# Performance work log

Measured on AMD Instinct MI355X. Metric: run time of the kernel, lower is better.

Reference implementation:

```python
import jax, jax.numpy as jnp
import numpy as np

HIDDEN = 2048
NUM_EXPERTS = 64
TOP_K = 8
EPS = 1e-6


def setup_inputs() -> dict:
    key = jax.random.key(0)
    k1, k2, k3, k4 = jax.random.split(key, 4)
    hidden_states = jax.random.normal(k1, (4, 4096, HIDDEN), dtype=jnp.float32)
    scale = jnp.ones((HIDDEN,), dtype=jnp.float32) + 0.01 * jax.random.normal(k2, (HIDDEN,), dtype=jnp.float32)
    proj_w = jax.random.normal(k3, (NUM_EXPERTS, HIDDEN), dtype=jnp.float32) * (HIDDEN ** -0.5)
    per_expert_scale = jnp.ones((NUM_EXPERTS,), dtype=jnp.float32) + 0.01 * jax.random.normal(k4, (NUM_EXPERTS,), dtype=jnp.float32)
    return {"hidden_states": hidden_states, "scale": scale, "proj_w": proj_w, "per_expert_scale": per_expert_scale}


def reference(hidden_states, scale, proj_w, per_expert_scale):
    H = hidden_states.shape[-1]
    # RMSNorm without learned scale
    x = hidden_states * jax.lax.rsqrt(jnp.mean(hidden_states * hidden_states, axis=-1, keepdims=True) + EPS)
    # elementwise scale and 1/sqrt(H) root-size scaling
    x = x * scale * (H ** -0.5)
    # router logits: [B,S,E]
    logits = jnp.einsum("bsh,eh->bse", x, proj_w)
    router_probs = jax.nn.softmax(logits.astype(jnp.float32), axis=-1)
    top_k_weights, top_k_index = jax.lax.top_k(router_probs, TOP_K)
    top_k_weights = top_k_weights / jnp.sum(top_k_weights, axis=-1, keepdims=True)
    top_k_weights = top_k_weights * per_expert_scale[top_k_index]
    # histc with bins=E, min=0, max=E on integer indices == bincount
    num_tokens_per_expert = jnp.bincount(top_k_index.reshape(-1), length=NUM_EXPERTS).astype(jnp.float32)
    return (top_k_weights.astype(hidden_states.dtype), top_k_index, num_tokens_per_expert)
```

## Files before the change

### kernel.cpp

```cpp
#include <hip/hip_runtime.h>
#include <math.h>

#define HIDDEN   2048
#define NEXPERT  64
#define TOPK     8
#define TILEK    64
#define LDSTR    68
#define RSQRT_H  0.02209708691207961f
#define NTOK     16384
#define EPW      4

__global__ __launch_bounds__(256) void prep_wt4(
    const float* __restrict__ w, const float* __restrict__ scale,
    float* __restrict__ wt4)
{
    int i  = blockIdx.x * 256 + threadIdx.x;
    int ep = i & 3;
    int k  = (i >> 2) & (HIDDEN - 1);
    int eg = i >> 13;
    wt4[i] = w[(eg * EPW + ep) * HIDDEN + k] * scale[k] * RSQRT_H;
}

__global__ __launch_bounds__(1024) void router_main(
    const float* __restrict__ h, const float* __restrict__ wt4,
    const float* __restrict__ pes,
    float* __restrict__ out_w, float* __restrict__ out_i, float* __restrict__ out_c)
{
    __shared__ float lds[2 * 64 * LDSTR];

    const int tid  = (int)threadIdx.x;
    const int wave = __builtin_amdgcn_readfirstlane(tid >> 6);
    const int lane = tid & 63;
    const int t0   = (int)blockIdx.x * 64;

    const int tt = tid >> 4;
    const int kk = (tid & 15) * 4;
    const float* __restrict__ hload = h + (size_t)(t0 + tt) * HIDDEN + kk;
    const int wtt = tt * LDSTR + kk;
    const int rdo = lane * LDSTR;

    const float* __restrict__ wbase = wt4 + (size_t)wave * (HIDDEN * EPW);

    double accd[EPW];
#pragma unroll
    for (int e = 0; e < EPW; ++e) accd[e] = 0.0;
    float ssl = 0.f;

    float4 v = *(const float4*)hload;

    for (int tile = 0; tile < HIDDEN / TILEK; ++tile) {
        float* buf = &lds[(tile & 1) * (64 * LDSTR)];
        *(float4*)(&buf[wtt]) = v;
        ssl = fmaf(v.x, v.x, ssl);
        ssl = fmaf(v.y, v.y, ssl);
        ssl = fmaf(v.z, v.z, ssl);
        ssl = fmaf(v.w, v.w, ssl);
        __syncthreads();
        if (tile < HIDDEN / TILEK - 1)
            v = *(const float4*)(hload + (tile + 1) * TILEK);

        const float* __restrict__ wk0 = wbase + tile * (TILEK * EPW);
        float acc[EPW];
#pragma unroll
        for (int e = 0; e < EPW; ++e) acc[e] = 0.f;
#pragma unroll
        for (int k4 = 0; k4 < TILEK; k4 += 4) {
            float4 h4 = *(const float4*)(&buf[rdo + k4]);
            const float* __restrict__ wk = wk0 + k4 * EPW;
#pragma unroll
            for (int e = 0; e < EPW; ++e) acc[e] = fmaf(wk[e],           h4.x, acc[e]);
#pragma unroll
            for (int e = 0; e < EPW; ++e) acc[e] = fmaf(wk[EPW + e],     h4.y, acc[e]);
#pragma unroll
            for (int e = 0; e < EPW; ++e) acc[e] = fmaf(wk[2 * EPW + e], h4.z, acc[e]);
#pragma unroll
            for (int e = 0; e < EPW; ++e) acc[e] = fmaf(wk[3 * EPW + e], h4.w, acc[e]);
        }
#pragma unroll
        for (int e = 0; e < EPW; ++e) accd[e] += (double)acc[e];
    }

    ssl += __shfl_xor(ssl, 1, 16);
    ssl += __shfl_xor(ssl, 2, 16);
    ssl += __shfl_xor(ssl, 4, 16);
    ssl += __shfl_xor(ssl, 8, 16);

    __syncthreads();
    float* lg   = lds;
    float* lss  = lds + 64 * 65;
    int*   hist = (int*)(lds + 64 * 65 + 64);
    if ((tid & 15) == 0) lss[tt] = ssl;
    if (tid < NEXPERT) hist[tid] = 0;
    __syncthreads();

    {
        float s = lss[lane];
        float r = (float)(1.0 / sqrt((double)s * (1.0 / (double)HIDDEN) + 1e-6));
#pragma unroll
        for (int e = 0; e < EPW; ++e)
            lg[lane * 65 + wave * EPW + e] = (float)accd[e] * r;
    }
    __syncthreads();

    for (int i = 0; i < 4; ++i) {
        const int tok = wave * 4 + i;
        float logit = lg[tok * 65 + lane];

        float work = logit;
        float myval = 0.f; int myidx = 0; float m0 = 0.f;
#pragma unroll
        for (int j = 0; j < TOPK; ++j) {
            float mx = work;
#pragma unroll
            for (int off = 32; off; off >>= 1) mx = fmaxf(mx, __shfl_xor(mx, off, 64));
            unsigned long long msk = __ballot(work == mx);
            int src = __ffsll((long long)msk) - 1;
            if (j == 0) m0 = mx;
            if (lane == j) { myval = mx; myidx = src; }
            if (lane == src) work = -3.402823466e38f;
        }

        float ev = (lane < TOPK) ? expf(myval - m0) : 0.f;
        float es = ev;
        es += __shfl_xor(es, 1, 64);
        es += __shfl_xor(es, 2, 64);
        es += __shfl_xor(es, 4, 64);
        if (lane < TOPK) {
            float wgt = (ev / es) * pes[myidx];
            size_t o = (size_t)(t0 + tok) * TOPK + lane;
            out_w[o] = wgt;
            out_i[o] = (float)myidx;
            atomicAdd(&hist[myidx], 1);
        }
    }

    __syncthreads();
    if (tid < NEXPERT)
        atomicAdd(&out_c[tid], (float)hist[tid]);
}

extern "C" void kernel_launch(void* const* d_in, const int* in_sizes, int n_in,
                              void* d_out, int out_size, void* d_ws, size_t ws_size,
                              hipStream_t stream) {
    const float* h     = (const float*)d_in[0];
    const float* scale = (const float*)d_in[1];
    const float* w     = (const float*)d_in[2];
    const float* pes   = (const float*)d_in[3];

    float* wt4 = (float*)d_ws;

    float* out_w = (float*)d_out;
    float* out_i = (float*)d_out + (size_t)NTOK * TOPK;
    float* out_c = (float*)d_out + (size_t)NTOK * TOPK * 2;

    hipMemsetAsync(out_c, 0, NEXPERT * sizeof(float), stream);

    prep_wt4<<<(NEXPERT * HIDDEN) / 256, 256, 0, stream>>>(w, scale, wt4);

    router_main<<<NTOK / 64, 1024, 0, stream>>>(h, wt4, pes, out_w, out_i, out_c);
}
```

Measured before the change: 254.8 us.

## Compute router logits with split-fp16 MFMA instead of scalar FP32 FMAs

Replaces the scalar FP32 FMA router GEMM with MFMA 16x16x32 f16 instructions. Both activations and weights are split into high and low fp16 parts, and three MFMAs per tile (hh, hl, lh) approximate fp32 precision. Blocks shrink to 16 tokens and 256 threads with a double-buffered LDS staging of converted activations. Each wave handles a K-slice, and the partial sums are reduced across waves through LDS before top-k. This removes the ALU-bound FMA cost so the kernel becomes bound by HBM reads of the hidden states. The trade-off is conversion overhead and a small precision change that could flip near-tie top-k selections.

```diff
diff --git a/kernel.cpp b/kernel.cpp
--- a/kernel.cpp
+++ b/kernel.cpp
@@ -4,107 +4,168 @@
 #define HIDDEN   2048
 #define NEXPERT  64
 #define TOPK     8
-#define TILEK    64
-#define LDSTR    68
-#define RSQRT_H  0.02209708691207961f
 #define NTOK     16384
-#define EPW      4
-
-__global__ __launch_bounds__(256) void prep_wt4(
+#define TOKB     16
+#define CHUNK    256
+#define NCHUNK   8
+#define ROWP     264
+#define RSQRT_H  0.02209708691207961
+#define WSCALE   64.0f
+
+typedef __attribute__((ext_vector_type(8))) _Float16 v8h;
+typedef __attribute__((ext_vector_type(4))) float    v4f;
+
+static __device__ __forceinline__ unsigned short f16b(float x) {
+    return __builtin_bit_cast(unsigned short, (_Float16)x);
+}
+static __device__ __forceinline__ float f16f(unsigned short u) {
+    return (float)__builtin_bit_cast(_Float16, u);
+}
+
+__global__ __launch_bounds__(256) void prep_wf(
     const float* __restrict__ w, const float* __restrict__ scale,
-    float* __restrict__ wt4)
+    unsigned short* __restrict__ wf)
 {
-    int i  = blockIdx.x * 256 + threadIdx.x;
-    int ep = i & 3;
-    int k  = (i >> 2) & (HIDDEN - 1);
-    int eg = i >> 13;
-    wt4[i] = w[(eg * EPW + ep) * HIDDEN + k] * scale[k] * RSQRT_H;
-}
-
-__global__ __launch_bounds__(1024) void router_main(
-    const float* __restrict__ h, const float* __restrict__ wt4,
+    int i    = blockIdx.x * 256 + threadIdx.x;
+    int j    = i & 7;
+    int lane = (i >> 3) & 63;
+    int nt   = (i >> 9) & 3;
+    int ks   = i >> 11;
+    int e    = nt * 16 + (lane & 15);
+    int k    = ks * 32 + (lane >> 4) * 8 + j;
+    float v  = w[e * HIDDEN + k] * scale[k] * WSCALE;
+    unsigned short vh = f16b(v);
+    unsigned short vl = f16b(v - f16f(vh));
+    size_t base = (((size_t)(ks * 4 + nt) * 2) * 64 + lane) * 8 + j;
+    wf[base]       = vh;
+    wf[base + 512] = vl;
+}
+
+__global__ __launch_bounds__(256, 4) void router_main(
+    const float* __restrict__ h, const unsigned short* __restrict__ wf,
     const float* __restrict__ pes,
     float* __restrict__ out_w, float* __restrict__ out_i, float* __restrict__ out_c)
 {
-    __shared__ float lds[2 * 64 * LDSTR];
+    __shared__ __align__(16) char smem[34112];
+    unsigned short* Xb0 = (unsigned short*)smem;
+    float* lss = (float*)(smem + 33792);
+    int*   hist = (int*)(smem + 33856);
+    float* lg  = (float*)smem;
 
     const int tid  = (int)threadIdx.x;
-    const int wave = __builtin_amdgcn_readfirstlane(tid >> 6);
+    const int w    = __builtin_amdgcn_readfirstlane(tid >> 6);
     const int lane = tid & 63;
-    const int t0   = (int)blockIdx.x * 64;
-
-    const int tt = tid >> 4;
-    const int kk = (tid & 15) * 4;
-    const float* __restrict__ hload = h + (size_t)(t0 + tt) * HIDDEN + kk;
-    const int wtt = tt * LDSTR + kk;
-    const int rdo = lane * LDSTR;
-
-    const float* __restrict__ wbase = wt4 + (size_t)wave * (HIDDEN * EPW);
-
-    double accd[EPW];
-#pragma unroll
-    for (int e = 0; e < EPW; ++e) accd[e] = 0.0;
-    float ssl = 0.f;
-
-    float4 v = *(const float4*)hload;
-
-    for (int tile = 0; tile < HIDDEN / TILEK; ++tile) {
-        float* buf = &lds[(tile & 1) * (64 * LDSTR)];
-        *(float4*)(&buf[wtt]) = v;
-        ssl = fmaf(v.x, v.x, ssl);
-        ssl = fmaf(v.y, v.y, ssl);
-        ssl = fmaf(v.z, v.z, ssl);
-        ssl = fmaf(v.w, v.w, ssl);
+    const int m    = lane & 15;
+    const int quad = lane >> 4;
+    const int t0   = (int)blockIdx.x * TOKB;
+
+    if (tid < NEXPERT) hist[tid] = 0;
+
+    const int aoff = m * ROWP + quad * 8;
+
+    v4f acc[4];
+#pragma unroll
+    for (int nt = 0; nt < 4; ++nt) acc[nt] = (v4f)0.f;
+    float ss[4] = {0.f, 0.f, 0.f, 0.f};
+    float4 st[4];
+
+#pragma unroll
+    for (int i = 0; i < 4; ++i) {
+        int idx = i * 256 + tid, t = idx >> 6, kq = idx & 63;
+        st[i] = *(const float4*)(h + (size_t)(t0 + t) * HIDDEN + kq * 4);
+    }
+#pragma unroll
+    for (int i = 0; i < 4; ++i) {
+        int idx = i * 256 + tid, t = idx >> 6, kq = idx & 63;
+        float4 v = st[i];
+        ss[i] = fmaf(v.x, v.x, fmaf(v.y, v.y, fmaf(v.z, v.z, fmaf(v.w, v.w, ss[i]))));
+        unsigned short h0 = f16b(v.x), h1 = f16b(v.y), h2 = f16b(v.z), h3 = f16b(v.w);
+        unsigned short l0 = f16b(v.x - f16f(h0)), l1 = f16b(v.y - f16f(h1));
+        unsigned short l2 = f16b(v.z - f16f(h2)), l3 = f16b(v.w - f16f(h3));
+        uint2 hp = make_uint2((unsigned)h0 | ((unsigned)h1 << 16),
+                              (unsigned)h2 | ((unsigned)h3 << 16));
+        uint2 lp = make_uint2((unsigned)l0 | ((unsigned)l1 << 16),
+                              (unsigned)l2 | ((unsigned)l3 << 16));
+        *(uint2*)(&Xb0[t * ROWP + kq * 4])        = hp;
+        *(uint2*)(&Xb0[4224 + t * ROWP + kq * 4]) = lp;
+    }
+
+    for (int c = 0; c < NCHUNK; ++c) {
         __syncthreads();
-        if (tile < HIDDEN / TILEK - 1)
-            v = *(const float4*)(hload + (tile + 1) * TILEK);
-
-        const float* __restrict__ wk0 = wbase + tile * (TILEK * EPW);
-        float acc[EPW];
-#pragma unroll
-        for (int e = 0; e < EPW; ++e) acc[e] = 0.f;
-#pragma unroll
-        for (int k4 = 0; k4 < TILEK; k4 += 4) {
-            float4 h4 = *(const float4*)(&buf[rdo + k4]);
-            const float* __restrict__ wk = wk0 + k4 * EPW;
-#pragma unroll
-            for (int e = 0; e < EPW; ++e) acc[e] = fmaf(wk[e],           h4.x, acc[e]);
-#pragma unroll
-            for (int e = 0; e < EPW; ++e) acc[e] = fmaf(wk[EPW + e],     h4.y, acc[e]);
-#pragma unroll
-            for (int e = 0; e < EPW; ++e) acc[e] = fmaf(wk[2 * EPW + e], h4.z, acc[e]);
-#pragma unroll
-            for (int e = 0; e < EPW; ++e) acc[e] = fmaf(wk[3 * EPW + e], h4.w, acc[e]);
-        }
-#pragma unroll
-        for (int e = 0; e < EPW; ++e) accd[e] += (double)acc[e];
-    }
-
-    ssl += __shfl_xor(ssl, 1, 16);
-    ssl += __shfl_xor(ssl, 2, 16);
-    ssl += __shfl_xor(ssl, 4, 16);
-    ssl += __shfl_xor(ssl, 8, 16);
-
+        unsigned short* buf = Xb0 + (c & 1) * 8448;
+        unsigned short* nbuf = Xb0 + ((c + 1) & 1) * 8448;
+
+        if (c < NCHUNK - 1) {
+#pragma unroll
+            for (int i = 0; i < 4; ++i) {
+                int idx = i * 256 + tid, t = idx >> 6, kq = idx & 63;
+                st[i] = *(const float4*)(h + (size_t)(t0 + t) * HIDDEN
+                                           + (c + 1) * CHUNK + kq * 4);
+            }
+        }
+
+#pragma unroll
+        for (int s = 0; s < 2; ++s) {
+            const int ksl = 2 * w + s;
+            const int ksg = c * 8 + ksl;
+            v8h ah = *(const v8h*)(&buf[aoff + ksl * 32]);
+            v8h al = *(const v8h*)(&buf[4224 + aoff + ksl * 32]);
+#pragma unroll
+            for (int nt = 0; nt < 4; ++nt) {
+                const unsigned short* bp =
+                    wf + (((size_t)(ksg * 4 + nt) * 2) * 64 + lane) * 8;
+                v8h bh = *(const v8h*)bp;
+                v8h bl = *(const v8h*)(bp + 512);
+                acc[nt] = __builtin_amdgcn_mfma_f32_16x16x32_f16(ah, bh, acc[nt], 0, 0, 0);
+                acc[nt] = __builtin_amdgcn_mfma_f32_16x16x32_f16(ah, bl, acc[nt], 0, 0, 0);
+                acc[nt] = __builtin_amdgcn_mfma_f32_16x16x32_f16(al, bh, acc[nt], 0, 0, 0);
+            }
+        }
+
+        if (c < NCHUNK - 1) {
+#pragma unroll
+            for (int i = 0; i < 4; ++i) {
+                int idx = i * 256 + tid, t = idx >> 6, kq = idx & 63;
+                float4 v = st[i];
+                ss[i] = fmaf(v.x, v.x, fmaf(v.y, v.y, fmaf(v.z, v.z, fmaf(v.w, v.w, ss[i]))));
+                unsigned short h0 = f16b(v.x), h1 = f16b(v.y), h2 = f16b(v.z), h3 = f16b(v.w);
+                unsigned short l0 = f16b(v.x - f16f(h0)), l1 = f16b(v.y - f16f(h1));
+                unsigned short l2 = f16b(v.z - f16f(h2)), l3 = f16b(v.w - f16f(h3));
+                uint2 hp = make_uint2((unsigned)h0 | ((unsigned)h1 << 16),
+                                      (unsigned)h2 | ((unsigned)h3 << 16));
+                uint2 lp = make_uint2((unsigned)l0 | ((unsigned)l1 << 16),
+                                      (unsigned)l2 | ((unsigned)l3 << 16));
+                *(uint2*)(&nbuf[t * ROWP + kq * 4])        = hp;
+                *(uint2*)(&nbuf[4224 + t * ROWP + kq * 4]) = lp;
+            }
+        }
+    }
+
+#pragma unroll
+    for (int i = 0; i < 4; ++i) {
+        float s = ss[i];
+#pragma unroll
+        for (int off = 32; off; off >>= 1) s += __shfl_xor(s, off, 64);
+        if (lane == 0) lss[i * 4 + w] = s;
+    }
     __syncthreads();
-    float* lg   = lds;
-    float* lss  = lds + 64 * 65;
-    int*   hist = (int*)(lds + 64 * 65 + 64);
-    if ((tid & 15) == 0) lss[tt] = ssl;
-    if (tid < NEXPERT) hist[tid] = 0;
+
+#pragma unroll
+    for (int nt = 0; nt < 4; ++nt)
+#pragma unroll
+        for (int r = 0; r < 4; ++r) {
+            int tl = quad * 4 + r;
+            lg[(w * 16 + tl) * 65 + nt * 16 + m] = acc[nt][r];
+        }
     __syncthreads();
 
-    {
-        float s = lss[lane];
-        float r = (float)(1.0 / sqrt((double)s * (1.0 / (double)HIDDEN) + 1e-6));
-#pragma unroll
-        for (int e = 0; e < EPW; ++e)
-            lg[lane * 65 + wave * EPW + e] = (float)accd[e] * r;
-    }
-    __syncthreads();
-
-    for (int i = 0; i < 4; ++i) {
-        const int tok = wave * 4 + i;
-        float logit = lg[tok * 65 + lane];
+    for (int i = 0; i < 4; ++i) {
+        const int tok = w * 4 + i;
+        float lsum = (lg[tok * 65 + lane]          + lg[1040 + tok * 65 + lane])
+                   + (lg[2080 + tok * 65 + lane]   + lg[3120 + tok * 65 + lane]);
+        double sst = (double)lss[tok];
+        double rr  = 1.0 / sqrt(sst * (1.0 / (double)HIDDEN) + 1e-6);
+        float logit = (float)((double)lsum * rr * (RSQRT_H / (double)WSCALE));
 
         float work = logit;
         float myval = 0.f; int myidx = 0; float m0 = 0.f;
@@ -147,7 +208,7 @@
     const float* w     = (const float*)d_in[2];
     const float* pes   = (const float*)d_in[3];
 
-    float* wt4 = (float*)d_ws;
+    unsigned short* wf = (unsigned short*)d_ws;
 
     float* out_w = (float*)d_out;
     float* out_i = (float*)d_out + (size_t)NTOK * TOPK;
@@ -155,7 +216,7 @@
 
     hipMemsetAsync(out_c, 0, NEXPERT * sizeof(float), stream);
 
-    prep_wt4<<<(NEXPERT * HIDDEN) / 256, 256, 0, stream>>>(w, scale, wt4);
-
-    router_main<<<NTOK / 64, 1024, 0, stream>>>(h, wt4, pes, out_w, out_i, out_c);
-}
+    prep_wf<<<512, 256, 0, stream>>>(w, scale, wf);
+
+    router_main<<<NTOK / TOKB, 256, 0, stream>>>(h, wf, pes, out_w, out_i, out_c);
+}
```

Result: faster. 234.5 us (-8.0%).
